# Kernel tuning notes

Measured on AMD Instinct MI355X. Metric: run time of the kernel, lower is better.

The kernel has to match this reference:

```python
import jax, jax.numpy as jnp
import numpy as np

D_MODEL = 1024
D_ATTN = 1024
N_HEADS = 16
D_FF = 4096
EPS = 1e-6


def _ln(x, gamma, beta):
    # Matches the custom LayerNorm: (x - mean) / (std + eps), std = sqrt(biased var)
    mean = jnp.mean(x, axis=-1, keepdims=True)
    std = jnp.sqrt(jnp.mean((x - mean) ** 2, axis=-1, keepdims=True))
    return gamma * ((x - mean) / (std + EPS)) + beta


def setup_inputs() -> dict:
    key = jax.random.key(0)
    ks = jax.random.split(key, 16)
    s = 0.02
    d, da, dff = D_MODEL, D_ATTN, D_FF
    inp = {
        "x": jax.random.normal(ks[0], (1, 2048, d), dtype=jnp.float32),
        "g1": jnp.ones((d,), jnp.float32),
        "beta1": jnp.zeros((d,), jnp.float32),
        "W_in": jax.random.normal(ks[1], (d, da), jnp.float32) * s,
        "b_in": jnp.zeros((da,), jnp.float32),
        "Wq": jax.random.normal(ks[2], (da, da), jnp.float32) * s,
        "bq": jnp.zeros((da,), jnp.float32),
        "Wk": jax.random.normal(ks[3], (da, da), jnp.float32) * s,
        "bk": jnp.zeros((da,), jnp.float32),
        "Wv": jax.random.normal(ks[4], (da, da), jnp.float32) * s,
        "bv": jnp.zeros((da,), jnp.float32),
        "Wo": jax.random.normal(ks[5], (da, da), jnp.float32) * s,
        "bo": jnp.zeros((da,), jnp.float32),
        "W2": jax.random.normal(ks[6], (da, d), jnp.float32) * s,
        "b2": jnp.zeros((d,), jnp.float32),
        "g2": jnp.ones((d,), jnp.float32),
        "beta2": jnp.zeros((d,), jnp.float32),
        "Wf1": jax.random.normal(ks[7], (d, dff), jnp.float32) * s,
        "bf1": jnp.zeros((dff,), jnp.float32),
        "Wf2": jax.random.normal(ks[8], (dff, d), jnp.float32) * s,
        "bf2": jnp.zeros((d,), jnp.float32),
    }
    return inp


def reference(x, g1, beta1, W_in, b_in, Wq, bq, Wk, bk, Wv, bv, Wo, bo,
              W2, b2, g2, beta2, Wf1, bf1, Wf2, bf2):
    B, S, _ = x.shape
    H, dk = N_HEADS, D_ATTN // N_HEADS

    norm_x = _ln(x, g1, beta1)
    h = norm_x @ W_in + b_in                      # [B,S,d_attn]

    def split_heads(t):
        return t.reshape(B, S, H, dk).transpose(0, 2, 1, 3)  # [B,H,S,dk]

    q = split_heads(h @ Wq + bq)
    k = split_heads(h @ Wk + bk)
    v = split_heads(h @ Wv + bv)

    scores = jnp.einsum("bhqd,bhkd->bhqk", q, k) / jnp.sqrt(jnp.float32(dk))
    causal = jnp.tril(jnp.ones((S, S), bool))[None, None]
    scores = jnp.where(causal, scores, -jnp.inf)
    attn_weights = jax.nn.softmax(scores, axis=-1)            # [B,H,S,S]
    ctx = jnp.einsum("bhqk,bhkd->bhqd", attn_weights, v)
    ctx = ctx.transpose(0, 2, 1, 3).reshape(B, S, D_ATTN)
    mha_out = ctx @ Wo + bo

    part1 = x + (mha_out @ W2 + b2)
    norm2 = _ln(part1, g2, beta2)
    ff = jnp.maximum(norm2 @ Wf1 + bf1, 0.0) @ Wf2 + bf2
    out = norm2 + ff
    return out, attn_weights
```

## Files before the change

kernel.cpp:

```cpp
#include <hip/hip_runtime.h>
#include <hip/hip_bf16.h>
#include <cstdint>

#define S_LEN 2048
#define D_MOD 1024
#define N_HEADS 16
#define DK 64
#define D_FF 4096

typedef __bf16 bf16x8 __attribute__((ext_vector_type(8)));
typedef float f32x4 __attribute__((ext_vector_type(4)));

#define MFMA16(a, b, c) __builtin_amdgcn_mfma_f32_16x16x32_bf16((a), (b), (c), 0, 0, 0)

__device__ inline unsigned pack_bf16x2(float a, float b)
{
    unsigned short ua = __builtin_bit_cast(unsigned short, (__bf16)a);
    unsigned short ub = __builtin_bit_cast(unsigned short, (__bf16)b);
    return (unsigned)ua | ((unsigned)ub << 16);
}

__device__ inline void gload16(const void* g, void* l)
{
    __builtin_amdgcn_global_load_lds(
        (const __attribute__((address_space(1))) unsigned int*)g,
        (__attribute__((address_space(3))) unsigned int*)l, 16, 0, 0);
}

template<int BN, bool RELU, bool RES, bool RES2, bool WF32, bool WBF16>
__device__ __forceinline__
void gemm_dev(const __bf16* __restrict__ A, const __bf16* __restrict__ BT,
              const float* __restrict__ bias, const float* __restrict__ res,
              const float* __restrict__ res2,
              float* __restrict__ Cf, __bf16* __restrict__ Cb,
              int N, int Kst, int Klp, int bx, int by,
              uint4* As, uint4* Bs)
{
    constexpr int NFRAG = BN / 32;
    const int tid = threadIdx.x;
    const int lane = tid & 63;
    const int w = tid >> 6;
    const int lrow = lane & 15;
    const int g = lane >> 4;
    const int bm = by * 128;
    const int bn = bx * BN;
    const int wrow = (w >> 1) * 64;
    const int wcol = (w & 1) * (BN / 2);

    f32x4 acc[4][NFRAG];
    for (int m = 0; m < 4; m++)
        for (int n = 0; n < NFRAG; n++)
            acc[m][n] = (f32x4){0.f, 0.f, 0.f, 0.f};

    const int srow = tid >> 3;
    const int sc = tid & 7;
    const __bf16* Ag = A + (size_t)(bm + srow) * Kst + sc * 8;
    const __bf16* Bg = BT + (size_t)(bn + srow) * Kst + sc * 8;

    for (int kt = 0; kt < Klp; kt += 64) {
        __syncthreads();
        #pragma unroll
        for (int p = 0; p < 4; p++)
            gload16(Ag + (size_t)(p * 32) * Kst + kt, &As[(srow + p * 32) * 8 + sc]);
        #pragma unroll
        for (int p = 0; p < NFRAG; p++)
            gload16(Bg + (size_t)(p * 32) * Kst + kt, &Bs[(srow + p * 32) * 8 + sc]);
        asm volatile("s_waitcnt vmcnt(0)" ::: "memory");
        __syncthreads();
        #pragma unroll
        for (int kk = 0; kk < 2; kk++) {
            bf16x8 af[4], bfr[NFRAG];
            int c = kk * 4 + g;
            #pragma unroll
            for (int m = 0; m < 4; m++)
                af[m] = __builtin_bit_cast(bf16x8, As[(wrow + m * 16 + lrow) * 8 + c]);
            #pragma unroll
            for (int n = 0; n < NFRAG; n++)
                bfr[n] = __builtin_bit_cast(bf16x8, Bs[(wcol + n * 16 + lrow) * 8 + c]);
            #pragma unroll
            for (int m = 0; m < 4; m++)
                #pragma unroll
                for (int n = 0; n < NFRAG; n++)
                    acc[m][n] = MFMA16(af[m], bfr[n], acc[m][n]);
        }
    }

    for (int n = 0; n < NFRAG; n++) {
        int col = bn + wcol + n * 16 + lrow;
        float bval = bias ? bias[col] : 0.f;
        for (int m = 0; m < 4; m++) {
            int row0 = bm + wrow + m * 16 + g * 4;
            for (int r = 0; r < 4; r++) {
                int row = row0 + r;
                float v = acc[m][n][r] + bval;
                if (RELU) v = fmaxf(v, 0.f);
                if (RES) v += res[(size_t)row * N + col];
                if (RES2) v += res2[(size_t)row * N + col];
                if (WF32) Cf[(size_t)row * N + col] = v;
                if (WBF16) Cb[(size_t)row * N + col] = (__bf16)v;
            }
        }
    }
}

__device__ __forceinline__
void ln_row(int row, const float* __restrict__ x, const float* __restrict__ gamma,
            const float* __restrict__ beta, __bf16* __restrict__ outb,
            float* __restrict__ outf, float* red)
{
    int tid = threadIdx.x;
    const float4 v = ((const float4*)(x + (size_t)row * D_MOD))[tid];
    float s = v.x + v.y + v.z + v.w;
    float sq = v.x * v.x + v.y * v.y + v.z * v.z + v.w * v.w;
    for (int off = 32; off; off >>= 1) {
        s += __shfl_down(s, off);
        sq += __shfl_down(sq, off);
    }
    int wid = tid >> 6;
    if ((tid & 63) == 0) { red[wid] = s; red[wid + 4] = sq; }
    __syncthreads();
    s = red[0] + red[1] + red[2] + red[3];
    sq = red[4] + red[5] + red[6] + red[7];
    float mean = s * (1.f / D_MOD);
    float var = fmaxf(sq * (1.f / D_MOD) - mean * mean, 0.f);
    float inv = 1.f / (sqrtf(var) + 1e-6f);
    float4 gv = ((const float4*)gamma)[tid];
    float4 bv = ((const float4*)beta)[tid];
    float y0 = gv.x * ((v.x - mean) * inv) + bv.x;
    float y1 = gv.y * ((v.y - mean) * inv) + bv.y;
    float y2 = gv.z * ((v.z - mean) * inv) + bv.z;
    float y3 = gv.w * ((v.w - mean) * inv) + bv.w;
    uint2 pk;
    pk.x = pack_bf16x2(y0, y1);
    pk.y = pack_bf16x2(y2, y3);
    ((uint2*)(outb + (size_t)row * D_MOD))[tid] = pk;
    if (outf) {
        float4 o = {y0, y1, y2, y3};
        ((float4*)(outf + (size_t)row * D_MOD))[tid] = o;
    }
}

__device__ __forceinline__
void pwrite_tile(const __bf16* __restrict__ qkv, const float* __restrict__ Obuf,
                 float* __restrict__ P, int h, int qt, int kt)
{
    const int tid = threadIdx.x;
    const int lane = tid & 63;
    const int w = tid >> 6;
    const int lrow = lane & 15;
    const int g = lane >> 4;
    const float c1 = 0.18033688f;
    const __bf16* ksec = qkv + 1024;
    const size_t Pb = (size_t)h * S_LEN * S_LEN;

    bf16x8 qfr[2][2];
    #pragma unroll
    for (int qq = 0; qq < 2; qq++)
        #pragma unroll
        for (int kk = 0; kk < 2; kk++)
            qfr[qq][kk] = *(const bf16x8*)(qkv +
                (size_t)(qt * 128 + w * 32 + qq * 16 + lrow) * 3072 + h * DK + kk * 32 + g * 8);

    f32x4 acc[2][8];
    #pragma unroll
    for (int qq = 0; qq < 2; qq++)
        #pragma unroll
        for (int mf = 0; mf < 8; mf++) acc[qq][mf] = (f32x4){0.f, 0.f, 0.f, 0.f};
    #pragma unroll
    for (int kk = 0; kk < 2; kk++) {
        #pragma unroll
        for (int mf = 0; mf < 8; mf++) {
            bf16x8 kf = *(const bf16x8*)(ksec +
                (size_t)(kt * 128 + mf * 16 + lrow) * 3072 + h * DK + kk * 32 + g * 8);
            acc[0][mf] = MFMA16(kf, qfr[0][kk], acc[0][mf]);
            acc[1][mf] = MFMA16(kf, qfr[1][kk], acc[1][mf]);
        }
    }

    #pragma unroll
    for (int qq = 0; qq < 2; qq++) {
        int q = qt * 128 + w * 32 + qq * 16 + lrow;
        float offv = Obuf[h * S_LEN + q];
        float* prow = P + Pb + (size_t)q * S_LEN;
        if (kt == qt) {
            #pragma unroll
            for (int mf = 0; mf < 8; mf++) {
                int kvb = kt * 128 + mf * 16 + g * 4;
                f32x4 st;
                st[0] = (kvb + 0 <= q) ? exp2f(acc[qq][mf][0] * c1 + offv) : 0.f;
                st[1] = (kvb + 1 <= q) ? exp2f(acc[qq][mf][1] * c1 + offv) : 0.f;
                st[2] = (kvb + 2 <= q) ? exp2f(acc[qq][mf][2] * c1 + offv) : 0.f;
                st[3] = (kvb + 3 <= q) ? exp2f(acc[qq][mf][3] * c1 + offv) : 0.f;
                __builtin_nontemporal_store(st, (f32x4*)(prow + kvb));
            }
        } else {
            #pragma unroll
            for (int mf = 0; mf < 8; mf++) {
                int kvb = kt * 128 + mf * 16 + g * 4;
                f32x4 st;
                st[0] = exp2f(acc[qq][mf][0] * c1 + offv);
                st[1] = exp2f(acc[qq][mf][1] * c1 + offv);
                st[2] = exp2f(acc[qq][mf][2] * c1 + offv);
                st[3] = exp2f(acc[qq][mf][3] * c1 + offv);
                __builtin_nontemporal_store(st, (f32x4*)(prow + kvb));
            }
        }
    }
}

__global__ __launch_bounds__(256)
void prep1(const float* __restrict__ Wq, const float* __restrict__ Wk,
           const float* __restrict__ Wv, const float* __restrict__ W2,
           const float* __restrict__ Wf1, const float* __restrict__ Wf2,
           const float* __restrict__ W_in, const float* __restrict__ Wo,
           const float* __restrict__ b_in, const float* __restrict__ bo,
           __bf16* __restrict__ WqkvT, __bf16* __restrict__ W2T,
           __bf16* __restrict__ Wf1T, __bf16* __restrict__ Wf2T,
           __bf16* __restrict__ Win_b, __bf16* __restrict__ Wo_b,
           float* __restrict__ part)
{
    __shared__ float tile[32][33];
    int id = blockIdx.x;
    int tid = threadIdx.x;
    if (id < 12288) {
        const float* W; __bf16* WT; int K, N, n0, k0;
        if (id < 4096) {
            int m = id >> 10; id &= 1023;
            K = 1024; N = 1024;
            n0 = (id & 31) * 32; k0 = (id >> 5) * 32;
            W = m == 0 ? Wq : (m == 1 ? Wk : (m == 2 ? Wv : W2));
            WT = m == 3 ? W2T : WqkvT + (size_t)m * 1024 * 1024;
        } else if (id < 8192) {
            id -= 4096;
            K = 1024; N = 4096;
            n0 = (id & 127) * 32; k0 = (id >> 7) * 32;
            W = Wf1; WT = Wf1T;
        } else {
            id -= 8192;
            K = 4096; N = 1024;
            n0 = (id & 31) * 32; k0 = (id >> 5) * 32;
            W = Wf2; WT = Wf2T;
        }
        int tx = tid & 31, ty = tid >> 5;
        for (int i = 0; i < 4; i++)
            tile[ty + i * 8][tx] = W[(size_t)(k0 + ty + i * 8) * N + n0 + tx];
        __syncthreads();
        for (int i = 0; i < 4; i++)
            WT[(size_t)(n0 + ty + i * 8) * K + k0 + tx] = (__bf16)tile[tx][ty + i * 8];
        return;
    }
    id -= 12288;
    if (id < 2048) {
        const float* W = id < 1024 ? W_in : Wo;
        __bf16* o = id < 1024 ? Win_b : Wo_b;
        int i = (id & 1023) * 256 + tid;
        float4 v = ((const float4*)W)[i];
        uint2 pk;
        pk.x = pack_bf16x2(v.x, v.y);
        pk.y = pack_bf16x2(v.z, v.w);
        ((uint2*)o)[i] = pk;
        return;
    }
    id -= 2048;
    {
        int n = (id & 15) * 256 + tid;
        int kc = id >> 4;
        int sel = n >> 10, col = n & 1023;
        const float* W = sel == 0 ? Wq : (sel == 1 ? Wk : (sel == 2 ? Wv : W2));
        const float* src = sel < 3 ? b_in : bo;
        float s = 0.f;
        for (int k = kc * 128; k < kc * 128 + 128; k++)
            s += src[k] * W[(size_t)k * 1024 + col];
        part[kc * 4096 + n] = s;
    }
}

__global__ __launch_bounds__(256, 2)
void prep2(const __bf16* __restrict__ WqkvT, const __bf16* __restrict__ Win_b,
           __bf16* __restrict__ WqkvCT,
           const __bf16* __restrict__ W2T, const __bf16* __restrict__ Wo_b,
           __bf16* __restrict__ WcombT,
           const float* __restrict__ part,
           const float* __restrict__ bq, const float* __restrict__ bk,
           const float* __restrict__ bv, const float* __restrict__ b2,
           float* __restrict__ bqkv, float* __restrict__ bcomb,
           const float* __restrict__ x, const float* __restrict__ g1,
           const float* __restrict__ beta1, __bf16* __restrict__ xn_b)
{
    __shared__ uint4 As[128 * 8];
    __shared__ uint4 Bs[64 * 8];
    int id = blockIdx.x;
    int tid = threadIdx.x;
    if (id < 384) {
        gemm_dev<64, false, false, false, false, true>(
            WqkvT, Win_b, nullptr, nullptr, nullptr, nullptr, WqkvCT,
            1024, 1024, 1024, id & 15, id >> 4, As, Bs);
        return;
    }
    id -= 384;
    if (id < 128) {
        gemm_dev<64, false, false, false, false, true>(
            W2T, Wo_b, nullptr, nullptr, nullptr, nullptr, WcombT,
            1024, 1024, 1024, id & 15, id >> 4, As, Bs);
        return;
    }
    id -= 128;
    if (id < 16) {
        int n = id * 256 + tid;
        int sel = n >> 10, col = n & 1023;
        float s = sel == 0 ? bq[col] : (sel == 1 ? bk[col] : (sel == 2 ? bv[col] : b2[col]));
        for (int kc = 0; kc < 8; kc++) s += part[kc * 4096 + n];
        if (n < 3072) bqkv[n] = s; else bcomb[col] = s;
        return;
    }
    id -= 16;
    ln_row(id, x, g1, beta1, xn_b, nullptr, (float*)As);
}

template<int BN, bool RELU, bool RES, bool RES2, bool WF32, bool WBF16>
__global__ __launch_bounds__(256, 2)
void gemm_kernel(const __bf16* __restrict__ A, const __bf16* __restrict__ BT,
                 const float* __restrict__ bias, const float* __restrict__ res,
                 const float* __restrict__ res2,
                 float* __restrict__ Cf, __bf16* __restrict__ Cb,
                 int N, int Kst, int Klp)
{
    __shared__ uint4 As[128 * 8];
    __shared__ uint4 Bs[BN * 8];
    gemm_dev<BN, RELU, RES, RES2, WF32, WBF16>(
        A, BT, bias, res, res2, Cf, Cb, N, Kst, Klp,
        blockIdx.x, blockIdx.y, As, Bs);
}

__global__ __launch_bounds__(256)
void vhead_transpose(const __bf16* __restrict__ v, __bf16* __restrict__ vt)
{
    __shared__ __bf16 tile[32][33];
    int tx = threadIdx.x & 31, ty = threadIdx.x >> 5;
    int s0 = blockIdx.x * 32;
    int d0 = blockIdx.y * 32;
    int h = blockIdx.z;
    for (int i = 0; i < 4; i++)
        tile[ty + i * 8][tx] = v[(size_t)(s0 + ty + i * 8) * 3072 + h * DK + d0 + tx];
    __syncthreads();
    for (int i = 0; i < 4; i++)
        vt[(size_t)(h * DK + d0 + ty + i * 8) * S_LEN + s0 + tx] = tile[tx][ty + i * 8];
}

__global__ __launch_bounds__(256)
void ln_kernel(const float* __restrict__ x, const float* __restrict__ gamma,
               const float* __restrict__ beta, __bf16* __restrict__ outb,
               float* __restrict__ outf)
{
    __shared__ float red[8];
    ln_row(blockIdx.x, x, gamma, beta, outb, outf, red);
}

__global__ __launch_bounds__(256, 3)
void attn_flash(const __bf16* __restrict__ qkv, const __bf16* __restrict__ vt,
                float* __restrict__ Obuf, __bf16* __restrict__ ctx,
                float* __restrict__ P)
{
    __shared__ char Ks[16384];
    __shared__ char Vs[16384];
    __shared__ char Plds[4][4096];
    const int tid = threadIdx.x;

    if (blockIdx.x >= 512) {
        int id = blockIdx.x - 512;
        int h = id / 120;
        int pr = id - h * 120;
        int qt = 0, acc = 0;
        while (pr >= acc + 15 - qt) { acc += 15 - qt; qt++; }
        int kt = qt + 1 + (pr - acc);
        f32x4 z = {0.f, 0.f, 0.f, 0.f};
        float* base = P + (size_t)h * S_LEN * S_LEN + (size_t)(qt * 128) * S_LEN + kt * 128;
        #pragma unroll
        for (int i = 0; i < 16; i++) {
            int idx = i * 256 + tid;
            int row = idx >> 5, c = idx & 31;
            __builtin_nontemporal_store(z, (f32x4*)(base + (size_t)row * S_LEN + c * 4));
        }
        return;
    }

    const int lane = tid & 63;
    const int w = tid >> 6;
    const int lrow = lane & 15;
    const int g = lane >> 4;
    const int h = blockIdx.x & 15;
    const int b = 31 - ((int)blockIdx.x >> 4);
    const int qg = b * 64 + w * 16 + lrow;
    const int ntiles = (b >> 1) + 1;
    const float c1 = 0.18033688f;
    const __bf16* ksec = qkv + 1024;
    char* plB = Plds[w];

    bf16x8 qf[2];
    qf[0] = *(const bf16x8*)(qkv + (size_t)qg * 3072 + h * DK + g * 8);
    qf[1] = *(const bf16x8*)(qkv + (size_t)qg * 3072 + h * DK + 32 + g * 8);

    float m2 = -1e30f, l = 0.f;
    f32x4 acc2[4];
    #pragma unroll
    for (int i = 0; i < 4; i++) acc2[i] = (f32x4){0.f, 0.f, 0.f, 0.f};

    const int sKrow = (w << 3) + (lane >> 3);
    const int sKch = lane & 7;
    const int sVrow = (w << 2) + (lane >> 4);
    const int sVch = lane & 15;
    char* const KsW = Ks + w * 1024;
    char* const VsW = Vs + w * 1024;

    for (int kt = 0; kt < ntiles; kt++) {
        #pragma unroll
        for (int p = 0; p < 4; p++) {
            int row = sKrow + p * 32;
            int ch = sKch ^ (row & 7);
            gload16(ksec + (size_t)(kt * 128 + row) * 3072 + h * DK + ch * 8,
                    KsW + p * 4096 + lane * 16);
        }
        #pragma unroll
        for (int p = 0; p < 4; p++) {
            int row = sVrow + p * 16;
            int ch = sVch ^ (row & 7);
            gload16(vt + (size_t)(h * DK + row) * S_LEN + kt * 128 + ch * 8,
                    VsW + p * 4096 + lane * 16);
        }
        asm volatile("s_waitcnt vmcnt(0)" ::: "memory");
        __syncthreads();

        f32x4 acc[8];
        #pragma unroll
        for (int mf = 0; mf < 8; mf++) acc[mf] = (f32x4){0.f, 0.f, 0.f, 0.f};
        #pragma unroll
        for (int kk = 0; kk < 2; kk++)
            #pragma unroll
            for (int mf = 0; mf < 8; mf++) {
                int row = mf * 16 + lrow;
                bf16x8 kf = *(const bf16x8*)(Ks + row * 128 + (((kk * 4 + g) ^ (row & 7)) << 4));
                acc[mf] = MFMA16(kf, qf[kk], acc[mf]);
            }

        float s[8][4];
        float tmx = -1e30f;
        const bool lastT = (kt == ntiles - 1);
        #pragma unroll
        for (int mf = 0; mf < 8; mf++) {
            int kvb = kt * 128 + mf * 16 + g * 4;
            #pragma unroll
            for (int r = 0; r < 4; r++) {
                float sv = acc[mf][r] * c1;
                if (lastT) sv = (kvb + r <= qg) ? sv : -1e30f;
                s[mf][r] = sv;
                tmx = fmaxf(tmx, sv);
            }
        }
        if (!__all((int)(tmx <= m2 + 6.f))) {
            float tm = fmaxf(tmx, __shfl_xor(tmx, 16));
            tm = fmaxf(tm, __shfl_xor(tm, 32));
            float nm = fmaxf(m2, tm);
            float sc = exp2f(m2 - nm);
            l *= sc;
            #pragma unroll
            for (int md = 0; md < 4; md++) acc2[md] *= sc;
            m2 = nm;
        }
        float sum = 0.f;
        #pragma unroll
        for (int mf = 0; mf < 8; mf++) {
            float p0 = exp2f(s[mf][0] - m2);
            float p1 = exp2f(s[mf][1] - m2);
            float p2 = exp2f(s[mf][2] - m2);
            float p3 = exp2f(s[mf][3] - m2);
            sum += (p0 + p1) + (p2 + p3);
            uint2 pk;
            pk.x = pack_bf16x2(p0, p1);
            pk.y = pack_bf16x2(p2, p3);
            *(uint2*)(plB + ((lrow * 256 + mf * 32 + g * 8) ^ ((lrow & 7) << 4))) = pk;
        }
        l += sum;

        #pragma unroll
        for (int ks = 0; ks < 4; ks++) {
            bf16x8 pf = *(bf16x8*)(plB + ((lrow * 256 + ks * 64 + g * 16) ^ ((lrow & 7) << 4)));
            #pragma unroll
            for (int md = 0; md < 4; md++) {
                int row = md * 16 + lrow;
                bf16x8 vf = *(const bf16x8*)(Vs + row * 256 + (((ks * 4 + g) ^ (row & 7)) << 4));
                acc2[md] = MFMA16(vf, pf, acc2[md]);
            }
        }
        __syncthreads();
    }

    l += __shfl_xor(l, 16);
    l += __shfl_xor(l, 32);
    float li = 1.f / l;
    if (lane < 16)
        Obuf[h * S_LEN + qg] = -m2 - log2f(l);
    #pragma unroll
    for (int md = 0; md < 4; md++) {
        uint2 pk;
        pk.x = pack_bf16x2(acc2[md][0] * li, acc2[md][1] * li);
        pk.y = pack_bf16x2(acc2[md][2] * li, acc2[md][3] * li);
        *(uint2*)(ctx + (size_t)qg * D_MOD + h * DK + md * 16 + g * 4) = pk;
    }
}

__global__ __launch_bounds__(256)
void ff1_pwrite(const __bf16* __restrict__ A, const __bf16* __restrict__ BT,
                const float* __restrict__ bias, __bf16* __restrict__ Cb,
                const __bf16* __restrict__ qkv, const float* __restrict__ Obuf,
                float* __restrict__ P)
{
    __shared__ uint4 As[128 * 8];
    __shared__ uint4 Bs[128 * 8];
    if (blockIdx.x < 512) {
        int bid = blockIdx.x;
        gemm_dev<128, true, false, false, false, true>(
            A, BT, bias, nullptr, nullptr, nullptr, Cb,
            D_FF, 1024, 1024, bid & 31, bid >> 5, As, Bs);
        return;
    }
    int idp = blockIdx.x - 512;
    int h = idp / 136;
    int tt = idp - h * 136;
    int qt = 0;
    while (tt > qt) { tt -= qt + 1; qt++; }
    pwrite_tile(qkv, Obuf, P, h, qt, tt);
}

__global__ __launch_bounds__(256)
void ff2_pwrite(const __bf16* __restrict__ ff1_b, const __bf16* __restrict__ Wf2T,
                float* __restrict__ partA, float* __restrict__ partB,
                const __bf16* __restrict__ qkv, const float* __restrict__ Obuf,
                float* __restrict__ P)
{
    __shared__ uint4 As[128 * 8];
    __shared__ uint4 Bs[64 * 8];
    if (blockIdx.x < 512) {
        int half = blockIdx.x >> 8;
        int b2 = blockIdx.x & 255;
        const __bf16* Ah = ff1_b + half * 2048;
        const __bf16* Bh = Wf2T + half * 2048;
        float* Cf = half ? partB : partA;
        gemm_dev<64, false, false, false, true, false>(
            Ah, Bh, nullptr, nullptr, nullptr, Cf, nullptr,
            1024, 4096, 2048, b2 & 15, b2 >> 4, As, Bs);
        return;
    }
    int idp = blockIdx.x - 512;
    int h = 8 + idp / 136;
    int tt = idp - (idp / 136) * 136;
    int qt = 0;
    while (tt > qt) { tt -= qt + 1; qt++; }
    pwrite_tile(qkv, Obuf, P, h, qt, tt);
}

__global__ __launch_bounds__(256)
void ff2_reduce(const float* __restrict__ partA, const float* __restrict__ partB,
                const float* __restrict__ norm2f, const float* __restrict__ bf2,
                float* __restrict__ outp)
{
    int idx = blockIdx.x * 256 + threadIdx.x;
    int col = (idx * 4) & 1023;
    f32x4 a = *(const f32x4*)(partA + (size_t)idx * 4);
    f32x4 b = *(const f32x4*)(partB + (size_t)idx * 4);
    f32x4 n = *(const f32x4*)(norm2f + (size_t)idx * 4);
    f32x4 bb = *(const f32x4*)(bf2 + col);
    f32x4 o = a + b + n + bb;
    *(f32x4*)(outp + (size_t)idx * 4) = o;
}

extern "C" void kernel_launch(void* const* d_in, const int* in_sizes, int n_in,
                              void* d_out, int out_size, void* d_ws, size_t ws_size,
                              hipStream_t stream)
{
    const float* x     = (const float*)d_in[0];
    const float* g1    = (const float*)d_in[1];
    const float* beta1 = (const float*)d_in[2];
    const float* W_in  = (const float*)d_in[3];
    const float* b_in  = (const float*)d_in[4];
    const float* Wq    = (const float*)d_in[5];
    const float* bq    = (const float*)d_in[6];
    const float* Wk    = (const float*)d_in[7];
    const float* bk    = (const float*)d_in[8];
    const float* Wv    = (const float*)d_in[9];
    const float* bv    = (const float*)d_in[10];
    const float* Wo    = (const float*)d_in[11];
    const float* bo    = (const float*)d_in[12];
    const float* W2    = (const float*)d_in[13];
    const float* b2    = (const float*)d_in[14];
    const float* g2    = (const float*)d_in[15];
    const float* beta2 = (const float*)d_in[16];
    const float* Wf1   = (const float*)d_in[17];
    const float* bf1   = (const float*)d_in[18];
    const float* Wf2   = (const float*)d_in[19];
    const float* bf2   = (const float*)d_in[20];

    float* outp = (float*)d_out;
    float* Pout = outp + (size_t)S_LEN * D_MOD;

    char* p = (char*)d_ws;
    auto alloc = [&](size_t b) -> void* {
        void* r = (void*)p;
        p += (b + 255) & ~(size_t)255;
        return r;
    };
    __bf16* WqkvT    = (__bf16*)alloc((size_t)3072 * 1024 * 2);
    __bf16* W2T      = (__bf16*)alloc((size_t)1024 * 1024 * 2);
    __bf16* Wf1T     = (__bf16*)alloc((size_t)D_FF * D_MOD * 2);
    __bf16* Wf2T     = (__bf16*)alloc((size_t)D_MOD * D_FF * 2);
    __bf16* WqkvCT   = (__bf16*)alloc((size_t)3072 * 1024 * 2);
    __bf16* WcombT   = (__bf16*)alloc((size_t)1024 * 1024 * 2);
    float*  bqkv     = (float*)alloc((size_t)3072 * 4);
    float*  bcomb    = (float*)alloc((size_t)1024 * 4);
    float*  biaspart = (float*)alloc((size_t)8 * 4096 * 4);
    __bf16* xn_b     = (__bf16*)alloc((size_t)S_LEN * D_MOD * 2);
    __bf16* qkv_b    = (__bf16*)alloc((size_t)S_LEN * 3072 * 2);
    __bf16* VT       = (__bf16*)alloc((size_t)N_HEADS * DK * S_LEN * 2);
    __bf16* ctx_b    = (__bf16*)alloc((size_t)S_LEN * D_MOD * 2);
    float*  part1f   = (float*)alloc((size_t)S_LEN * D_MOD * 4);
    float*  norm2f   = (float*)alloc((size_t)S_LEN * D_MOD * 4);
    __bf16* norm2b   = (__bf16*)alloc((size_t)S_LEN * D_MOD * 2);
    __bf16* ff1_b    = (__bf16*)alloc((size_t)S_LEN * D_FF * 2);
    float*  Obuf     = (float*)alloc((size_t)N_HEADS * S_LEN * 4);
    float*  ffpartB  = (float*)alloc((size_t)S_LEN * D_MOD * 4);
    __bf16* Win_b   = (__bf16*)part1f;
    __bf16* Wo_b    = (__bf16*)norm2f;
    float*  ffpartA = part1f;

    dim3 blk(256);

    prep1<<<dim3(14464), blk, 0, stream>>>(Wq, Wk, Wv, W2, Wf1, Wf2, W_in, Wo,
                                           b_in, bo, WqkvT, W2T, Wf1T, Wf2T,
                                           Win_b, Wo_b, biaspart);

    prep2<<<dim3(2576), blk, 0, stream>>>(WqkvT, Win_b, WqkvCT, W2T, Wo_b, WcombT,
                                          biaspart, bq, bk, bv, b2, bqkv, bcomb,
                                          x, g1, beta1, xn_b);

    gemm_kernel<128, false, false, false, false, true><<<dim3(24, 16), blk, 0, stream>>>(
        xn_b, WqkvCT, bqkv, nullptr, nullptr, nullptr, qkv_b, 3072, 1024, 1024);

    vhead_transpose<<<dim3(64, 2, 16), blk, 0, stream>>>(qkv_b + 2048, VT);

    attn_flash<<<dim3(512 + 1920), blk, 0, stream>>>(qkv_b, VT, Obuf, ctx_b, Pout);

    gemm_kernel<64, false, true, false, true, false><<<dim3(16, 16), blk, 0, stream>>>(
        ctx_b, WcombT, bcomb, x, nullptr, part1f, nullptr, 1024, 1024, 1024);

    ln_kernel<<<S_LEN, blk, 0, stream>>>(part1f, g2, beta2, norm2b, norm2f);

    ff1_pwrite<<<dim3(512 + 1088), blk, 0, stream>>>(
        norm2b, Wf1T, bf1, ff1_b, qkv_b, Obuf, Pout);

    ff2_pwrite<<<dim3(512 + 1088), blk, 0, stream>>>(
        ff1_b, Wf2T, ffpartA, ffpartB, qkv_b, Obuf, Pout);

    ff2_reduce<<<dim3(2048), blk, 0, stream>>>(ffpartA, ffpartB, norm2f, bf2, outp);
}
```

Measured before the change: 261.8 us.

## Fuse V transpose into QKV GEMM, split zero-fill, double-buffer attention K/V

The QKV GEMM epilogue now also writes the V part transposed into VT, which removes the separate vhead_transpose kernel. Half of the zero-fill blocks for the upper-triangular part of P move into the QKV launch so that work overlaps the GEMM. The flash-attention loop double-buffers its K/V LDS tiles and issues the next tile's loads before waiting on the current one. The extra LDS lowers occupancy from 3 to 2 blocks per CU, and the transposed V writes are small 8-byte strided stores.

```diff
diff --git a/kernel.cpp b/kernel.cpp
--- a/kernel.cpp
+++ b/kernel.cpp
@@ -27,12 +27,13 @@
         (__attribute__((address_space(3))) unsigned int*)l, 16, 0, 0);
 }
 
-template<int BN, bool RELU, bool RES, bool RES2, bool WF32, bool WBF16>
+template<int BN, bool RELU, bool RES, bool RES2, bool WF32, bool WBF16, bool WVT>
 __device__ __forceinline__
 void gemm_dev(const __bf16* __restrict__ A, const __bf16* __restrict__ BT,
               const float* __restrict__ bias, const float* __restrict__ res,
               const float* __restrict__ res2,
               float* __restrict__ Cf, __bf16* __restrict__ Cb,
+              __bf16* __restrict__ vt,
               int N, int Kst, int Klp, int bx, int by,
               uint4* As, uint4* Bs)
 {
@@ -90,14 +91,22 @@
         float bval = bias ? bias[col] : 0.f;
         for (int m = 0; m < 4; m++) {
             int row0 = bm + wrow + m * 16 + g * 4;
+            float vv[4];
             for (int r = 0; r < 4; r++) {
                 int row = row0 + r;
                 float v = acc[m][n][r] + bval;
                 if (RELU) v = fmaxf(v, 0.f);
                 if (RES) v += res[(size_t)row * N + col];
                 if (RES2) v += res2[(size_t)row * N + col];
+                vv[r] = v;
                 if (WF32) Cf[(size_t)row * N + col] = v;
                 if (WBF16) Cb[(size_t)row * N + col] = (__bf16)v;
+            }
+            if (WVT && col >= 2048) {
+                uint2 pk;
+                pk.x = pack_bf16x2(vv[0], vv[1]);
+                pk.y = pack_bf16x2(vv[2], vv[3]);
+                *(uint2*)(vt + (size_t)(col - 2048) * S_LEN + row0) = pk;
             }
         }
     }
@@ -208,6 +217,25 @@
     }
 }
 
+__device__ __forceinline__
+void zfill_tile(float* __restrict__ P, int zid)
+{
+    int tid = threadIdx.x;
+    int h = zid / 120;
+    int pr = zid - h * 120;
+    int qt = 0, acc = 0;
+    while (pr >= acc + 15 - qt) { acc += 15 - qt; qt++; }
+    int kt = qt + 1 + (pr - acc);
+    f32x4 z = {0.f, 0.f, 0.f, 0.f};
+    float* base = P + (size_t)h * S_LEN * S_LEN + (size_t)(qt * 128) * S_LEN + kt * 128;
+    #pragma unroll
+    for (int i = 0; i < 16; i++) {
+        int idx = i * 256 + tid;
+        int row = idx >> 5, c = idx & 31;
+        __builtin_nontemporal_store(z, (f32x4*)(base + (size_t)row * S_LEN + c * 4));
+    }
+}
+
 __global__ __launch_bounds__(256)
 void prep1(const float* __restrict__ Wq, const float* __restrict__ Wk,
            const float* __restrict__ Wv, const float* __restrict__ W2,
@@ -292,15 +320,15 @@
     int id = blockIdx.x;
     int tid = threadIdx.x;
     if (id < 384) {
-        gemm_dev<64, false, false, false, false, true>(
-            WqkvT, Win_b, nullptr, nullptr, nullptr, nullptr, WqkvCT,
+        gemm_dev<64, false, false, false, false, true, false>(
+            WqkvT, Win_b, nullptr, nullptr, nullptr, nullptr, WqkvCT, nullptr,
             1024, 1024, 1024, id & 15, id >> 4, As, Bs);
         return;
     }
     id -= 384;
     if (id < 128) {
-        gemm_dev<64, false, false, false, false, true>(
-            W2T, Wo_b, nullptr, nullptr, nullptr, nullptr, WcombT,
+        gemm_dev<64, false, false, false, false, true, false>(
+            W2T, Wo_b, nullptr, nullptr, nullptr, nullptr, WcombT, nullptr,
             1024, 1024, 1024, id & 15, id >> 4, As, Bs);
         return;
     }
@@ -317,6 +345,23 @@
     ln_row(id, x, g1, beta1, xn_b, nullptr, (float*)As);
 }
 
+__global__ __launch_bounds__(256, 2)
+void qkv_zf(const __bf16* __restrict__ xn_b, const __bf16* __restrict__ WqkvCT,
+            const float* __restrict__ bqkv, __bf16* __restrict__ qkv_b,
+            __bf16* __restrict__ vt, float* __restrict__ P)
+{
+    __shared__ uint4 As[128 * 8];
+    __shared__ uint4 Bs[128 * 8];
+    if (blockIdx.x < 384) {
+        int bid = blockIdx.x;
+        gemm_dev<128, false, false, false, false, true, true>(
+            xn_b, WqkvCT, bqkv, nullptr, nullptr, nullptr, qkv_b, vt,
+            3072, 1024, 1024, bid % 24, bid / 24, As, Bs);
+        return;
+    }
+    zfill_tile(P, blockIdx.x - 384);
+}
+
 template<int BN, bool RELU, bool RES, bool RES2, bool WF32, bool WBF16>
 __global__ __launch_bounds__(256, 2)
 void gemm_kernel(const __bf16* __restrict__ A, const __bf16* __restrict__ BT,
@@ -327,24 +372,9 @@
 {
     __shared__ uint4 As[128 * 8];
     __shared__ uint4 Bs[BN * 8];
-    gemm_dev<BN, RELU, RES, RES2, WF32, WBF16>(
-        A, BT, bias, res, res2, Cf, Cb, N, Kst, Klp,
+    gemm_dev<BN, RELU, RES, RES2, WF32, WBF16, false>(
+        A, BT, bias, res, res2, Cf, Cb, nullptr, N, Kst, Klp,
         blockIdx.x, blockIdx.y, As, Bs);
-}
-
-__global__ __launch_bounds__(256)
-void vhead_transpose(const __bf16* __restrict__ v, __bf16* __restrict__ vt)
-{
-    __shared__ __bf16 tile[32][33];
-    int tx = threadIdx.x & 31, ty = threadIdx.x >> 5;
-    int s0 = blockIdx.x * 32;
-    int d0 = blockIdx.y * 32;
-    int h = blockIdx.z;
-    for (int i = 0; i < 4; i++)
-        tile[ty + i * 8][tx] = v[(size_t)(s0 + ty + i * 8) * 3072 + h * DK + d0 + tx];
-    __syncthreads();
-    for (int i = 0; i < 4; i++)
-        vt[(size_t)(h * DK + d0 + ty + i * 8) * S_LEN + s0 + tx] = tile[tx][ty + i * 8];
 }
 
 __global__ __launch_bounds__(256)
@@ -356,31 +386,18 @@
     ln_row(blockIdx.x, x, gamma, beta, outb, outf, red);
 }
 
-__global__ __launch_bounds__(256, 3)
+__global__ __launch_bounds__(256, 2)
 void attn_flash(const __bf16* __restrict__ qkv, const __bf16* __restrict__ vt,
                 float* __restrict__ Obuf, __bf16* __restrict__ ctx,
                 float* __restrict__ P)
 {
-    __shared__ char Ks[16384];
-    __shared__ char Vs[16384];
+    __shared__ char Ks[2][16384];
+    __shared__ char Vs[2][16384];
     __shared__ char Plds[4][4096];
     const int tid = threadIdx.x;
 
     if (blockIdx.x >= 512) {
-        int id = blockIdx.x - 512;
-        int h = id / 120;
-        int pr = id - h * 120;
-        int qt = 0, acc = 0;
-        while (pr >= acc + 15 - qt) { acc += 15 - qt; qt++; }
-        int kt = qt + 1 + (pr - acc);
-        f32x4 z = {0.f, 0.f, 0.f, 0.f};
-        float* base = P + (size_t)h * S_LEN * S_LEN + (size_t)(qt * 128) * S_LEN + kt * 128;
-        #pragma unroll
-        for (int i = 0; i < 16; i++) {
-            int idx = i * 256 + tid;
-            int row = idx >> 5, c = idx & 31;
-            __builtin_nontemporal_store(z, (f32x4*)(base + (size_t)row * S_LEN + c * 4));
-        }
+        zfill_tile(P, 960 + (int)blockIdx.x - 512);
         return;
     }
 
@@ -409,10 +426,10 @@
     const int sKch = lane & 7;
     const int sVrow = (w << 2) + (lane >> 4);
     const int sVch = lane & 15;
-    char* const KsW = Ks + w * 1024;
-    char* const VsW = Vs + w * 1024;
-
-    for (int kt = 0; kt < ntiles; kt++) {
+
+    auto stage = [&](int kt, int tb) {
+        char* KsW = Ks[tb] + w * 1024;
+        char* VsW = Vs[tb] + w * 1024;
         #pragma unroll
         for (int p = 0; p < 4; p++) {
             int row = sKrow + p * 32;
@@ -427,8 +444,22 @@
             gload16(vt + (size_t)(h * DK + row) * S_LEN + kt * 128 + ch * 8,
                     VsW + p * 4096 + lane * 16);
         }
-        asm volatile("s_waitcnt vmcnt(0)" ::: "memory");
+    };
+
+    stage(0, 0);
+
+    for (int kt = 0; kt < ntiles; kt++) {
+        const int cur = kt & 1;
+        if (kt + 1 < ntiles) {
+            stage(kt + 1, cur ^ 1);
+            asm volatile("s_waitcnt vmcnt(8)" ::: "memory");
+        } else {
+            asm volatile("s_waitcnt vmcnt(0)" ::: "memory");
+        }
         __syncthreads();
+
+        const char* Ksb = Ks[cur];
+        const char* Vsb = Vs[cur];
 
         f32x4 acc[8];
         #pragma unroll
@@ -438,7 +469,7 @@
             #pragma unroll
             for (int mf = 0; mf < 8; mf++) {
                 int row = mf * 16 + lrow;
-                bf16x8 kf = *(const bf16x8*)(Ks + row * 128 + (((kk * 4 + g) ^ (row & 7)) << 4));
+                bf16x8 kf = *(const bf16x8*)(Ksb + row * 128 + (((kk * 4 + g) ^ (row & 7)) << 4));
                 acc[mf] = MFMA16(kf, qf[kk], acc[mf]);
             }
 
@@ -487,7 +518,7 @@
             #pragma unroll
             for (int md = 0; md < 4; md++) {
                 int row = md * 16 + lrow;
-                bf16x8 vf = *(const bf16x8*)(Vs + row * 256 + (((ks * 4 + g) ^ (row & 7)) << 4));
+                bf16x8 vf = *(const bf16x8*)(Vsb + row * 256 + (((ks * 4 + g) ^ (row & 7)) << 4));
                 acc2[md] = MFMA16(vf, pf, acc2[md]);
             }
         }
@@ -518,8 +549,8 @@
     __shared__ uint4 Bs[128 * 8];
     if (blockIdx.x < 512) {
         int bid = blockIdx.x;
-        gemm_dev<128, true, false, false, false, true>(
-            A, BT, bias, nullptr, nullptr, nullptr, Cb,
+        gemm_dev<128, true, false, false, false, true, false>(
+            A, BT, bias, nullptr, nullptr, nullptr, Cb, nullptr,
             D_FF, 1024, 1024, bid & 31, bid >> 5, As, Bs);
         return;
     }
@@ -545,8 +576,8 @@
         const __bf16* Ah = ff1_b + half * 2048;
         const __bf16* Bh = Wf2T + half * 2048;
         float* Cf = half ? partB : partA;
-        gemm_dev<64, false, false, false, true, false>(
-            Ah, Bh, nullptr, nullptr, nullptr, Cf, nullptr,
+        gemm_dev<64, false, false, false, true, false, false>(
+            Ah, Bh, nullptr, nullptr, nullptr, Cf, nullptr, nullptr,
             1024, 4096, 2048, b2 & 15, b2 >> 4, As, Bs);
         return;
     }
@@ -641,12 +672,9 @@
                                           biaspart, bq, bk, bv, b2, bqkv, bcomb,
                                           x, g1, beta1, xn_b);
 
-    gemm_kernel<128, false, false, false, false, true><<<dim3(24, 16), blk, 0, stream>>>(
-        xn_b, WqkvCT, bqkv, nullptr, nullptr, nullptr, qkv_b, 3072, 1024, 1024);
-
-    vhead_transpose<<<dim3(64, 2, 16), blk, 0, stream>>>(qkv_b + 2048, VT);
-
-    attn_flash<<<dim3(512 + 1920), blk, 0, stream>>>(qkv_b, VT, Obuf, ctx_b, Pout);
+    qkv_zf<<<dim3(384 + 960), blk, 0, stream>>>(xn_b, WqkvCT, bqkv, qkv_b, VT, Pout);
+
+    attn_flash<<<dim3(512 + 960), blk, 0, stream>>>(qkv_b, VT, Obuf, ctx_b, Pout);
 
     gemm_kernel<64, false, true, false, true, false><<<dim3(16, 16), blk, 0, stream>>>(
         ctx_b, WcombT, bcomb, x, nullptr, part1f, nullptr, 1024, 1024, 1024);
```

Result: no change. 260.2 us (-0.6%).
